# Performance work log

Hardware: AMD Instinct MI355X
Metric: run time of the kernel (lower is better)

Reference implementation:

```python
import jax, jax.numpy as jnp
import numpy as np

B, C, L, D = 16384, 4096, 2, 128  # batch, num_classes, len_label, hidden per prompt slot


def setup_inputs() -> dict:
    key = jax.random.key(0)
    k1, k2 = jax.random.split(key)
    batchs = jax.random.normal(k1, (B, L, D), dtype=jnp.float32)       # masked hidden states
    label2embed = jax.random.normal(k2, (C, L, D), dtype=jnp.float32)  # learned class prompts
    return {"batchs": batchs, "label2embed": label2embed}


def reference(batchs, label2embed):
    # Original ('mm' similarity):
    #   out[b, c] = sum(diag(batchs[b] @ label2embed[c].T))
    #             = sum_{p,d} batchs[b,p,d] * label2embed[c,p,d]
    # Fused row-wise dot product over the flattened (len_label, D) axes,
    # eliminating the O(L^2) mm+diag waste and the B*C Python loop.
    logits = jnp.einsum("bpd,cpd->bc", batchs, label2embed)  # [B, C]
    return logits
```

## Files before the change

### kernel.cpp

```cpp
#include <hip/hip_runtime.h>
#include <hip/hip_bf16.h>
#include <stdint.h>

#define MDIM 16384
#define NDIM 4096
#define KDIM 256

#define BM 128
#define BN 128
#define BK 32
#define KSTEPS (KDIM / BK)

typedef __attribute__((ext_vector_type(8))) short bf16x8;
typedef __attribute__((ext_vector_type(4))) float f32x4;

__device__ __forceinline__ unsigned short f2bf_rne(float f) {
    union { float f; uint32_t u; } v; v.f = f;
    uint32_t u = v.u;
    u += 0x7fffu + ((u >> 16) & 1u);
    return (unsigned short)(u >> 16);
}

__global__ __launch_bounds__(256) void cvt_kernel(const float* __restrict__ a,
                                                  const float* __restrict__ b,
                                                  unsigned short* __restrict__ wa,
                                                  unsigned short* __restrict__ wb) {
    const int64_t nA = (int64_t)MDIM * KDIM;
    int64_t i = ((int64_t)blockIdx.x * 256 + threadIdx.x) * 8;
    const float* src; unsigned short* dst; int64_t off;
    if (i < nA) { src = a; dst = wa; off = i; }
    else        { src = b; dst = wb; off = i - nA; }
    float4 f0 = *(const float4*)(src + off);
    float4 f1 = *(const float4*)(src + off + 4);
    union { unsigned short h[8]; int4 v; } o;
    o.h[0] = f2bf_rne(f0.x); o.h[1] = f2bf_rne(f0.y);
    o.h[2] = f2bf_rne(f0.z); o.h[3] = f2bf_rne(f0.w);
    o.h[4] = f2bf_rne(f1.x); o.h[5] = f2bf_rne(f1.y);
    o.h[6] = f2bf_rne(f1.z); o.h[7] = f2bf_rne(f1.w);
    *(int4*)(dst + off) = o.v;
}

__device__ __forceinline__ void stage_tiles(const unsigned short* __restrict__ Ab,
                                            const unsigned short* __restrict__ Bb,
                                            unsigned short* sA, unsigned short* sB,
                                            int tid, int k0) {
#pragma unroll
    for (int c = 0; c < 2; ++c) {
        int ch  = tid + c * 256;
        int row = ch >> 2;
        int col = (ch & 3) << 3;
        __builtin_amdgcn_global_load_lds(
            (const __attribute__((address_space(1))) void*)(Ab + (size_t)row * KDIM + k0 + col),
            (__attribute__((address_space(3))) void*)(sA + ch * 8), 16, 0, 0);
        __builtin_amdgcn_global_load_lds(
            (const __attribute__((address_space(1))) void*)(Bb + (size_t)row * KDIM + k0 + col),
            (__attribute__((address_space(3))) void*)(sB + ch * 8), 16, 0, 0);
    }
}

__global__ __launch_bounds__(256, 4) void gemm_bt(const unsigned short* __restrict__ A,
                                                  const unsigned short* __restrict__ Bm,
                                                  float* __restrict__ out) {
    __shared__ __align__(16) unsigned short sA[2][BM * BK];
    __shared__ __align__(16) unsigned short sB[2][BN * BK];

    const int tid  = threadIdx.x;
    const int lane = tid & 63;
    const int wave = tid >> 6;
    const int wm   = wave >> 1;
    const int wn   = wave & 1;

    const int id  = blockIdx.x;
    const int xcd = id & 7;
    const int g   = id >> 3;
    const int bm  = (xcd << 4) | (g >> 5);
    const int bn  = g & 31;

    const unsigned short* Ab = A  + (size_t)bm * BM * KDIM;
    const unsigned short* Bb = Bm + (size_t)bn * BN * KDIM;

    f32x4 acc[4][4] = {};

    const int quad = lane >> 4;
    const int r16  = lane & 15;

    stage_tiles(Ab, Bb, sA[0], sB[0], tid, 0);

#pragma unroll
    for (int step = 0; step < KSTEPS; ++step) {
        __syncthreads();
        if (step + 1 < KSTEPS)
            stage_tiles(Ab, Bb, sA[(step + 1) & 1], sB[(step + 1) & 1], tid, (step + 1) * BK);

        const unsigned short* cA = sA[step & 1];
        const unsigned short* cB = sB[step & 1];

        bf16x8 af[4], bf[4];
#pragma unroll
        for (int i = 0; i < 4; ++i)
            af[i] = *(const bf16x8*)(cA + ((wm * 64 + i * 16 + r16) * BK + quad * 8));
#pragma unroll
        for (int j = 0; j < 4; ++j)
            bf[j] = *(const bf16x8*)(cB + ((wn * 64 + j * 16 + r16) * BK + quad * 8));

#pragma unroll
        for (int i = 0; i < 4; ++i)
#pragma unroll
            for (int j = 0; j < 4; ++j)
                acc[i][j] = __builtin_amdgcn_mfma_f32_16x16x32_bf16(af[i], bf[j], acc[i][j], 0, 0, 0);
    }

#pragma unroll
    for (int i = 0; i < 4; ++i) {
        int rowb = bm * BM + wm * 64 + i * 16 + quad * 4;
#pragma unroll
        for (int j = 0; j < 4; ++j) {
            int colb = bn * BN + wn * 64 + j * 16 + r16;
            float* p = out + (size_t)rowb * NDIM + colb;
#pragma unroll
            for (int rr = 0; rr < 4; ++rr)
                p[(size_t)rr * NDIM] = acc[i][j][rr];
        }
    }
}

__global__ __launch_bounds__(256) void naive_f32(const float* __restrict__ a,
                                                 const float* __restrict__ b,
                                                 float* __restrict__ out) {
    int64_t idx = (int64_t)blockIdx.x * 256 + threadIdx.x;
    int c = (int)(idx & (NDIM - 1));
    int r = (int)(idx >> 12);
    const float4* ap = (const float4*)(a + (size_t)r * KDIM);
    const float4* bp = (const float4*)(b + (size_t)c * KDIM);
    float s = 0.f;
#pragma unroll 8
    for (int k = 0; k < KDIM / 4; ++k) {
        float4 x = ap[k], y = bp[k];
        s += x.x * y.x + x.y * y.y + x.z * y.z + x.w * y.w;
    }
    out[idx] = s;
}

extern "C" void kernel_launch(void* const* d_in, const int* in_sizes, int n_in,
                              void* d_out, int out_size, void* d_ws, size_t ws_size,
                              hipStream_t stream) {
    const float* a = (const float*)d_in[0];
    const float* b = (const float*)d_in[1];
    float* out = (float*)d_out;

    const size_t need = ((size_t)MDIM + NDIM) * KDIM * sizeof(unsigned short);
    if (d_ws != nullptr && ws_size >= need) {
        unsigned short* wa = (unsigned short*)d_ws;
        unsigned short* wb = wa + (size_t)MDIM * KDIM;
        const int64_t nvec = ((int64_t)MDIM + NDIM) * KDIM / 8;
        cvt_kernel<<<(int)(nvec / 256), 256, 0, stream>>>(a, b, wa, wb);
        gemm_bt<<<(MDIM / BM) * (NDIM / BN), 256, 0, stream>>>(wa, wb, out);
    } else {
        naive_f32<<<(int64_t)MDIM * NDIM / 256, 256, 0, stream>>>(a, b, out);
    }
}
```

Before: 297.0 us.

## Fuse fp32-to-bf16 conversion into GEMM with register-staged triple-buffered loads

Removes the separate conversion kernel and workspace round trip. The GEMM now loads fp32 tiles directly into registers, converts them to bf16 and writes them to a triple-buffered LDS ring while the MFMAs run. The MFMA operands are swapped so each lane holds four contiguous output columns, which allows 16-byte nontemporal vector stores. In exchange, every output tile block re-reads fp32 inputs (twice the bytes of bf16) and redoes the conversion, and occupancy drops to 3 blocks per CU.

```diff
diff --git a/kernel.cpp b/kernel.cpp
--- a/kernel.cpp
+++ b/kernel.cpp
@@ -1,5 +1,4 @@
 #include <hip/hip_runtime.h>
-#include <hip/hip_bf16.h>
 #include <stdint.h>
 
 #define MDIM 16384
@@ -13,6 +12,7 @@
 
 typedef __attribute__((ext_vector_type(8))) short bf16x8;
 typedef __attribute__((ext_vector_type(4))) float f32x4;
+typedef __attribute__((ext_vector_type(4))) unsigned short u16x4;
 
 __device__ __forceinline__ unsigned short f2bf_rne(float f) {
     union { float f; uint32_t u; } v; v.f = f;
@@ -21,54 +21,19 @@
     return (unsigned short)(u >> 16);
 }
 
-__global__ __launch_bounds__(256) void cvt_kernel(const float* __restrict__ a,
-                                                  const float* __restrict__ b,
-                                                  unsigned short* __restrict__ wa,
-                                                  unsigned short* __restrict__ wb) {
-    const int64_t nA = (int64_t)MDIM * KDIM;
-    int64_t i = ((int64_t)blockIdx.x * 256 + threadIdx.x) * 8;
-    const float* src; unsigned short* dst; int64_t off;
-    if (i < nA) { src = a; dst = wa; off = i; }
-    else        { src = b; dst = wb; off = i - nA; }
-    float4 f0 = *(const float4*)(src + off);
-    float4 f1 = *(const float4*)(src + off + 4);
-    union { unsigned short h[8]; int4 v; } o;
-    o.h[0] = f2bf_rne(f0.x); o.h[1] = f2bf_rne(f0.y);
-    o.h[2] = f2bf_rne(f0.z); o.h[3] = f2bf_rne(f0.w);
-    o.h[4] = f2bf_rne(f1.x); o.h[5] = f2bf_rne(f1.y);
-    o.h[6] = f2bf_rne(f1.z); o.h[7] = f2bf_rne(f1.w);
-    *(int4*)(dst + off) = o.v;
-}
-
-__device__ __forceinline__ void stage_tiles(const unsigned short* __restrict__ Ab,
-                                            const unsigned short* __restrict__ Bb,
-                                            unsigned short* sA, unsigned short* sB,
-                                            int tid, int k0) {
-#pragma unroll
-    for (int c = 0; c < 2; ++c) {
-        int ch  = tid + c * 256;
-        int row = ch >> 2;
-        int col = (ch & 3) << 3;
-        __builtin_amdgcn_global_load_lds(
-            (const __attribute__((address_space(1))) void*)(Ab + (size_t)row * KDIM + k0 + col),
-            (__attribute__((address_space(3))) void*)(sA + ch * 8), 16, 0, 0);
-        __builtin_amdgcn_global_load_lds(
-            (const __attribute__((address_space(1))) void*)(Bb + (size_t)row * KDIM + k0 + col),
-            (__attribute__((address_space(3))) void*)(sB + ch * 8), 16, 0, 0);
-    }
-}
-
-__global__ __launch_bounds__(256, 4) void gemm_bt(const unsigned short* __restrict__ A,
-                                                  const unsigned short* __restrict__ Bm,
-                                                  float* __restrict__ out) {
-    __shared__ __align__(16) unsigned short sA[2][BM * BK];
-    __shared__ __align__(16) unsigned short sB[2][BN * BK];
+__global__ __launch_bounds__(256, 3) void gemm_fused(const float* __restrict__ A,
+                                                     const float* __restrict__ Bm,
+                                                     float* __restrict__ out) {
+    __shared__ __align__(16) unsigned short sA[3][BM * BK];
+    __shared__ __align__(16) unsigned short sB[3][BN * BK];
 
     const int tid  = threadIdx.x;
     const int lane = tid & 63;
     const int wave = tid >> 6;
     const int wm   = wave >> 1;
     const int wn   = wave & 1;
+    const int quad = lane >> 4;
+    const int r16  = lane & 15;
 
     const int id  = blockIdx.x;
     const int xcd = id & 7;
@@ -76,69 +41,80 @@
     const int bm  = (xcd << 4) | (g >> 5);
     const int bn  = g & 31;
 
-    const unsigned short* Ab = A  + (size_t)bm * BM * KDIM;
-    const unsigned short* Bb = Bm + (size_t)bn * BN * KDIM;
+    const float* Ab = A  + (size_t)bm * BM * KDIM;
+    const float* Bb = Bm + (size_t)bn * BN * KDIM;
+
+    const int srow = tid >> 3;
+    const int scol = (tid & 7) << 2;
+
+    float4 pa[4], pb[4];
+
+    auto issueG = [&](int s) {
+#pragma unroll
+        for (int u = 0; u < 4; ++u)
+            pa[u] = *(const float4*)(Ab + (size_t)(srow + 32 * u) * KDIM + s * BK + scol);
+#pragma unroll
+        for (int u = 0; u < 4; ++u)
+            pb[u] = *(const float4*)(Bb + (size_t)(srow + 32 * u) * KDIM + s * BK + scol);
+    };
+
+    auto cvtWrite = [&](int buf) {
+        unsigned short* dA = &sA[buf][0];
+        unsigned short* dB = &sB[buf][0];
+#pragma unroll
+        for (int u = 0; u < 4; ++u) {
+            u16x4 ca, cb;
+            ca[0] = f2bf_rne(pa[u].x); ca[1] = f2bf_rne(pa[u].y);
+            ca[2] = f2bf_rne(pa[u].z); ca[3] = f2bf_rne(pa[u].w);
+            cb[0] = f2bf_rne(pb[u].x); cb[1] = f2bf_rne(pb[u].y);
+            cb[2] = f2bf_rne(pb[u].z); cb[3] = f2bf_rne(pb[u].w);
+            *(u16x4*)(dA + (size_t)tid * 4 + u * 1024) = ca;
+            *(u16x4*)(dB + (size_t)tid * 4 + u * 1024) = cb;
+        }
+    };
 
     f32x4 acc[4][4] = {};
 
-    const int quad = lane >> 4;
-    const int r16  = lane & 15;
-
-    stage_tiles(Ab, Bb, sA[0], sB[0], tid, 0);
+    issueG(0);
+    cvtWrite(0);
+    issueG(1);
+    __syncthreads();
 
 #pragma unroll
-    for (int step = 0; step < KSTEPS; ++step) {
-        __syncthreads();
-        if (step + 1 < KSTEPS)
-            stage_tiles(Ab, Bb, sA[(step + 1) & 1], sB[(step + 1) & 1], tid, (step + 1) * BK);
+    for (int s = 0; s < KSTEPS; ++s) {
+        const unsigned short* cA = sA[s % 3];
+        const unsigned short* cB = sB[s % 3];
 
-        const unsigned short* cA = sA[step & 1];
-        const unsigned short* cB = sB[step & 1];
-
-        bf16x8 af[4], bf[4];
+        bf16x8 af[4], bfr[4];
 #pragma unroll
         for (int i = 0; i < 4; ++i)
             af[i] = *(const bf16x8*)(cA + ((wm * 64 + i * 16 + r16) * BK + quad * 8));
 #pragma unroll
         for (int j = 0; j < 4; ++j)
-            bf[j] = *(const bf16x8*)(cB + ((wn * 64 + j * 16 + r16) * BK + quad * 8));
+            bfr[j] = *(const bf16x8*)(cB + ((wn * 64 + j * 16 + r16) * BK + quad * 8));
 
 #pragma unroll
         for (int i = 0; i < 4; ++i)
 #pragma unroll
             for (int j = 0; j < 4; ++j)
-                acc[i][j] = __builtin_amdgcn_mfma_f32_16x16x32_bf16(af[i], bf[j], acc[i][j], 0, 0, 0);
+                acc[i][j] = __builtin_amdgcn_mfma_f32_16x16x32_bf16(bfr[j], af[i], acc[i][j], 0, 0, 0);
+
+        if (s + 1 < KSTEPS) {
+            cvtWrite((s + 1) % 3);
+            if (s + 2 < KSTEPS) issueG(s + 2);
+        }
+        __syncthreads();
     }
 
 #pragma unroll
     for (int i = 0; i < 4; ++i) {
-        int rowb = bm * BM + wm * 64 + i * 16 + quad * 4;
+        size_t row = (size_t)bm * BM + wm * 64 + i * 16 + r16;
 #pragma unroll
         for (int j = 0; j < 4; ++j) {
-            int colb = bn * BN + wn * 64 + j * 16 + r16;
-            float* p = out + (size_t)rowb * NDIM + colb;
-#pragma unroll
-            for (int rr = 0; rr < 4; ++rr)
-                p[(size_t)rr * NDIM] = acc[i][j][rr];
+            int col = bn * BN + wn * 64 + j * 16 + quad * 4;
+            __builtin_nontemporal_store(acc[i][j], (f32x4*)(out + row * NDIM + col));
         }
     }
-}
-
-__global__ __launch_bounds__(256) void naive_f32(const float* __restrict__ a,
-                                                 const float* __restrict__ b,
-                                                 float* __restrict__ out) {
-    int64_t idx = (int64_t)blockIdx.x * 256 + threadIdx.x;
-    int c = (int)(idx & (NDIM - 1));
-    int r = (int)(idx >> 12);
-    const float4* ap = (const float4*)(a + (size_t)r * KDIM);
-    const float4* bp = (const float4*)(b + (size_t)c * KDIM);
-    float s = 0.f;
-#pragma unroll 8
-    for (int k = 0; k < KDIM / 4; ++k) {
-        float4 x = ap[k], y = bp[k];
-        s += x.x * y.x + x.y * y.y + x.z * y.z + x.w * y.w;
-    }
-    out[idx] = s;
 }
 
 extern "C" void kernel_launch(void* const* d_in, const int* in_sizes, int n_in,
@@ -147,15 +123,7 @@
     const float* a = (const float*)d_in[0];
     const float* b = (const float*)d_in[1];
     float* out = (float*)d_out;
+    (void)d_ws; (void)ws_size;
 
-    const size_t need = ((size_t)MDIM + NDIM) * KDIM * sizeof(unsigned short);
-    if (d_ws != nullptr && ws_size >= need) {
-        unsigned short* wa = (unsigned short*)d_ws;
-        unsigned short* wb = wa + (size_t)MDIM * KDIM;
-        const int64_t nvec = ((int64_t)MDIM + NDIM) * KDIM / 8;
-        cvt_kernel<<<(int)(nvec / 256), 256, 0, stream>>>(a, b, wa, wb);
-        gemm_bt<<<(MDIM / BM) * (NDIM / BN), 256, 0, stream>>>(wa, wb, out);
-    } else {
-        naive_f32<<<(int64_t)MDIM * NDIM / 256, 256, 0, stream>>>(a, b, out);
-    }
+    gemm_fused<<<(MDIM / BM) * (NDIM / BN), 256, 0, stream>>>(a, b, out);
 }
```

New measurement: 352.0 us. +18.5%, slower.

## Load MFMA fragments directly from global memory, drop LDS staging

Applied to the files above, without the earlier changes.

Replaces the LDS double-buffered tile staging with direct global loads of bf16 fragments into registers, which removes the __syncthreads barriers and the shared-memory traffic. The MFMA operands are swapped so each lane's accumulator holds four contiguous output columns, and the epilogue becomes a single 16-byte nontemporal vector store per fragment instead of four scalar strided stores. Operand reuse across waves now depends on L1/L2 caching rather than explicit LDS sharing, so global load traffic rises.

```diff
diff --git a/kernel.cpp b/kernel.cpp
--- a/kernel.cpp
+++ b/kernel.cpp
@@ -1,5 +1,4 @@
 #include <hip/hip_runtime.h>
-#include <hip/hip_bf16.h>
 #include <stdint.h>
 
 #define MDIM 16384
@@ -8,8 +7,6 @@
 
 #define BM 128
 #define BN 128
-#define BK 32
-#define KSTEPS (KDIM / BK)
 
 typedef __attribute__((ext_vector_type(8))) short bf16x8;
 typedef __attribute__((ext_vector_type(4))) float f32x4;
@@ -40,35 +37,16 @@
     *(int4*)(dst + off) = o.v;
 }
 
-__device__ __forceinline__ void stage_tiles(const unsigned short* __restrict__ Ab,
-                                            const unsigned short* __restrict__ Bb,
-                                            unsigned short* sA, unsigned short* sB,
-                                            int tid, int k0) {
-#pragma unroll
-    for (int c = 0; c < 2; ++c) {
-        int ch  = tid + c * 256;
-        int row = ch >> 2;
-        int col = (ch & 3) << 3;
-        __builtin_amdgcn_global_load_lds(
-            (const __attribute__((address_space(1))) void*)(Ab + (size_t)row * KDIM + k0 + col),
-            (__attribute__((address_space(3))) void*)(sA + ch * 8), 16, 0, 0);
-        __builtin_amdgcn_global_load_lds(
-            (const __attribute__((address_space(1))) void*)(Bb + (size_t)row * KDIM + k0 + col),
-            (__attribute__((address_space(3))) void*)(sB + ch * 8), 16, 0, 0);
-    }
-}
-
-__global__ __launch_bounds__(256, 4) void gemm_bt(const unsigned short* __restrict__ A,
-                                                  const unsigned short* __restrict__ Bm,
-                                                  float* __restrict__ out) {
-    __shared__ __align__(16) unsigned short sA[2][BM * BK];
-    __shared__ __align__(16) unsigned short sB[2][BN * BK];
-
+__global__ __launch_bounds__(256, 4) void gemm_direct(const unsigned short* __restrict__ A,
+                                                      const unsigned short* __restrict__ Bm,
+                                                      float* __restrict__ out) {
     const int tid  = threadIdx.x;
     const int lane = tid & 63;
     const int wave = tid >> 6;
     const int wm   = wave >> 1;
     const int wn   = wave & 1;
+    const int quad = lane >> 4;
+    const int r16  = lane & 15;
 
     const int id  = blockIdx.x;
     const int xcd = id & 7;
@@ -76,50 +54,35 @@
     const int bm  = (xcd << 4) | (g >> 5);
     const int bn  = g & 31;
 
-    const unsigned short* Ab = A  + (size_t)bm * BM * KDIM;
-    const unsigned short* Bb = Bm + (size_t)bn * BN * KDIM;
+    const unsigned short* Ab = A  + (size_t)(bm * BM + wm * 64 + r16) * KDIM + quad * 8;
+    const unsigned short* Bb = Bm + (size_t)(bn * BN + wn * 64 + r16) * KDIM + quad * 8;
 
     f32x4 acc[4][4] = {};
 
-    const int quad = lane >> 4;
-    const int r16  = lane & 15;
-
-    stage_tiles(Ab, Bb, sA[0], sB[0], tid, 0);
-
 #pragma unroll
-    for (int step = 0; step < KSTEPS; ++step) {
-        __syncthreads();
-        if (step + 1 < KSTEPS)
-            stage_tiles(Ab, Bb, sA[(step + 1) & 1], sB[(step + 1) & 1], tid, (step + 1) * BK);
-
-        const unsigned short* cA = sA[step & 1];
-        const unsigned short* cB = sB[step & 1];
-
-        bf16x8 af[4], bf[4];
+    for (int s = 0; s < KDIM / 32; ++s) {
+        bf16x8 af[4], bfr[4];
 #pragma unroll
         for (int i = 0; i < 4; ++i)
-            af[i] = *(const bf16x8*)(cA + ((wm * 64 + i * 16 + r16) * BK + quad * 8));
+            af[i] = *(const bf16x8*)(Ab + (size_t)i * 16 * KDIM + s * 32);
 #pragma unroll
         for (int j = 0; j < 4; ++j)
-            bf[j] = *(const bf16x8*)(cB + ((wn * 64 + j * 16 + r16) * BK + quad * 8));
+            bfr[j] = *(const bf16x8*)(Bb + (size_t)j * 16 * KDIM + s * 32);
 
 #pragma unroll
         for (int i = 0; i < 4; ++i)
 #pragma unroll
             for (int j = 0; j < 4; ++j)
-                acc[i][j] = __builtin_amdgcn_mfma_f32_16x16x32_bf16(af[i], bf[j], acc[i][j], 0, 0, 0);
+                acc[i][j] = __builtin_amdgcn_mfma_f32_16x16x32_bf16(bfr[j], af[i], acc[i][j], 0, 0, 0);
     }
 
 #pragma unroll
     for (int i = 0; i < 4; ++i) {
-        int rowb = bm * BM + wm * 64 + i * 16 + quad * 4;
+        size_t row = (size_t)bm * BM + wm * 64 + i * 16 + r16;
 #pragma unroll
         for (int j = 0; j < 4; ++j) {
-            int colb = bn * BN + wn * 64 + j * 16 + r16;
-            float* p = out + (size_t)rowb * NDIM + colb;
-#pragma unroll
-            for (int rr = 0; rr < 4; ++rr)
-                p[(size_t)rr * NDIM] = acc[i][j][rr];
+            int col = bn * BN + wn * 64 + j * 16 + quad * 4;
+            __builtin_nontemporal_store(acc[i][j], (f32x4*)(out + row * NDIM + col));
         }
     }
 }
@@ -154,7 +117,7 @@
         unsigned short* wb = wa + (size_t)MDIM * KDIM;
         const int64_t nvec = ((int64_t)MDIM + NDIM) * KDIM / 8;
         cvt_kernel<<<(int)(nvec / 256), 256, 0, stream>>>(a, b, wa, wb);
-        gemm_bt<<<(MDIM / BM) * (NDIM / BN), 256, 0, stream>>>(wa, wb, out);
+        gemm_direct<<<(MDIM / BM) * (NDIM / BN), 256, 0, stream>>>(wa, wb, out);
     } else {
         naive_f32<<<(int64_t)MDIM * NDIM / 256, 256, 0, stream>>>(a, b, out);
     }
```

After: 379.5 us. +27.8%, slower.
